# Kernel tuning notes

Hardware: AMD Instinct MI355X
Metric: run time of the kernel (lower is better)

## Reference

```python
import jax, jax.numpy as jnp
import numpy as np

N_NODES = 100000
N_EDGES = 1600000
IN_FEAT = 128
UNITS = 64


def setup_inputs() -> dict:
    key = jax.random.key(0)
    k1, k2, k3, k4, k5 = jax.random.split(key, 5)
    node_states = jax.random.normal(k1, (N_NODES, IN_FEAT), dtype=jnp.float32)
    # edges[:,0] is the destination/segment id; the original TF code's
    # repeat(bincount) normalization assumes edges sorted by edges[:,0].
    dst = jnp.sort(jax.random.randint(k2, (N_EDGES,), 0, N_NODES))
    src = jax.random.randint(k3, (N_EDGES,), 0, N_NODES)
    edges = jnp.stack([dst, src], axis=1).astype(jnp.int64)
    kernel = jax.random.normal(k4, (IN_FEAT, UNITS), dtype=jnp.float32) * 0.05
    kernel_attention = jax.random.normal(k5, (2 * UNITS, 1), dtype=jnp.float32) * 0.05
    return {"node_states": node_states, "edges": edges,
            "kernel": kernel, "kernel_attention": kernel_attention}


def reference(node_states, edges, kernel, kernel_attention):
    n_nodes = node_states.shape[0]
    dst = edges[:, 0]  # segment ids (aggregation target)
    src = edges[:, 1]  # neighbor being gathered

    h = node_states @ kernel                      # [N, U]
    h_dst = h[dst]                                # [E, U]
    h_src = h[src]                                # [E, U]
    # concat(h_dst, h_src) @ a  ==  h_dst @ a[:U] + h_src @ a[U:]
    u = kernel_attention.shape[0] // 2
    scores = (h_dst @ kernel_attention[:u] + h_src @ kernel_attention[u:])[:, 0]  # [E]
    scores = jax.nn.leaky_relu(scores, negative_slope=0.2)  # tf default alpha=0.2
    scores = jnp.exp(jnp.clip(scores, -2.0, 2.0))

    score_sum = jax.ops.segment_sum(scores, dst, num_segments=n_nodes)  # [N]
    attn = scores / score_sum[dst]                                      # [E]

    out = jax.ops.segment_sum(h_src * attn[:, None], dst, num_segments=n_nodes)  # [N, U]
    return out
```

## Files before the change

### kernel.cpp

```cpp
#include <hip/hip_runtime.h>
#include <hip/hip_bf16.h>

#define NN 100000
#define NE 1600000
#define NF 128
#define UU 64

typedef __attribute__((ext_vector_type(8))) short short8;
typedef __attribute__((ext_vector_type(4))) float f32x4;

static const size_t OFF_FLAG = 0;
static const size_t OFF_SRC  = 256;
static const size_t OFF_H2   = OFF_SRC + (size_t)NE * 4;
static const size_t OFF_AD   = OFF_H2  + (size_t)NN * UU * 2;
static const size_t OFF_AS   = OFF_AD  + (size_t)NN * 4;
static const size_t OFF_ROW  = OFF_AS  + (size_t)NN * 4;
static const size_t OFF_WP   = OFF_ROW + (size_t)(NN + 1) * 4;

__device__ __forceinline__ unsigned short bfr(float v) {
    unsigned u = __float_as_uint(v);
    return (unsigned short)((u + 0x7FFFu + ((u >> 16) & 1u)) >> 16);
}

__global__ __launch_bounds__(256) void prep(const int* __restrict__ ew,
                                            const float* __restrict__ W,
                                            int* __restrict__ flag,
                                            unsigned short* __restrict__ Wp) {
    if (threadIdx.x == 0) {
        int a = ew[2 * 400000 + 1] | ew[2 * 800000 + 1] |
                ew[2 * 1200000 + 1] | ew[2 * 1599999 + 1];
        *flag = (a == 0) ? 1 : 0;
    }
    for (int i = threadIdx.x; i < 8192; i += 256) {
        int j   = i & 7;
        int l15 = (i >> 3) & 15;
        int quad = (i >> 7) & 3;
        int kb  = (i >> 9) & 3;
        int nt  = i >> 11;
        Wp[i] = bfr(W[(size_t)(kb * 32 + quad * 8 + j) * UU + nt * 16 + l15]);
    }
}

#define GEMM_BLOCKS   1563
#define ROWS_BLOCKS   391
#define UNPACK_BLOCKS 1563

__global__ __launch_bounds__(256) void mega(const float* __restrict__ X,
                                            const void* __restrict__ edges,
                                            const int* __restrict__ flag,
                                            const unsigned short* __restrict__ Wp,
                                            const float* __restrict__ ka,
                                            unsigned short* __restrict__ h2,
                                            float* __restrict__ a_dst,
                                            float* __restrict__ a_src,
                                            int* __restrict__ src32,
                                            int* __restrict__ rows) {
    int bid = blockIdx.x;
    int tid = threadIdx.x;

    if (bid < GEMM_BLOCKS) {
        int wv = tid >> 6, lane = tid & 63;
        int quad = lane >> 4, l15 = lane & 15;
        int nb = bid * 64 + wv * 16;
        int row = nb + l15; if (row >= NN) row = NN - 1;
        const float* xr = X + (size_t)row * NF + quad * 8;

        short8 afrag[4];
#pragma unroll
        for (int kb = 0; kb < 4; kb++) {
            float4 p0 = *(const float4*)(xr + kb * 32);
            float4 p1 = *(const float4*)(xr + kb * 32 + 4);
            short8 a;
            a[0] = (short)bfr(p0.x); a[1] = (short)bfr(p0.y);
            a[2] = (short)bfr(p0.z); a[3] = (short)bfr(p0.w);
            a[4] = (short)bfr(p1.x); a[5] = (short)bfr(p1.y);
            a[6] = (short)bfr(p1.z); a[7] = (short)bfr(p1.w);
            afrag[kb] = a;
        }

        f32x4 acc[4] = {f32x4{0,0,0,0}, f32x4{0,0,0,0}, f32x4{0,0,0,0}, f32x4{0,0,0,0}};
        const short8* wpf = (const short8*)Wp;
#pragma unroll
        for (int nt = 0; nt < 4; nt++) {
#pragma unroll
            for (int kb = 0; kb < 4; kb++) {
                short8 b = wpf[((nt * 4 + kb) * 4 + quad) * 16 + l15];
                acc[nt] = __builtin_amdgcn_mfma_f32_16x16x32_bf16(afrag[kb], b, acc[nt], 0, 0, 0);
            }
        }

        float kad[4], kas[4];
#pragma unroll
        for (int nt = 0; nt < 4; nt++) {
            kad[nt] = ka[nt * 16 + l15];
            kas[nt] = ka[64 + nt * 16 + l15];
        }
#pragma unroll
        for (int r = 0; r < 4; r++) {
            int m = nb + quad * 4 + r;
            if (m < NN) {
#pragma unroll
                for (int nt = 0; nt < 4; nt++)
                    h2[(size_t)m * UU + nt * 16 + l15] = bfr(acc[nt][r]);
            }
            float pd = acc[0][r] * kad[0] + acc[1][r] * kad[1] + acc[2][r] * kad[2] + acc[3][r] * kad[3];
            float ps = acc[0][r] * kas[0] + acc[1][r] * kas[1] + acc[2][r] * kas[2] + acc[3][r] * kas[3];
            pd += __shfl_xor(pd, 1); pd += __shfl_xor(pd, 2);
            pd += __shfl_xor(pd, 4); pd += __shfl_xor(pd, 8);
            ps += __shfl_xor(ps, 1); ps += __shfl_xor(ps, 2);
            ps += __shfl_xor(ps, 4); ps += __shfl_xor(ps, 8);
            if (l15 == 0 && m < NN) { a_dst[m] = pd; a_src[m] = ps; }
        }
        return;
    }
    bid -= GEMM_BLOCKS;

    if (bid < ROWS_BLOCKS) {
        int n = bid * 256 + tid;
        if (n > NN) return;
        if (n == NN) { rows[NN] = NE; return; }
        int fl = *flag;
        const int* ew = (const int*)edges;
        int lo = 0, hi = NE;
        while (lo < hi) {
            int mid = (lo + hi) >> 1;
            int d = fl ? ew[4 * (size_t)mid] : ew[2 * (size_t)mid];
            if (d < n) lo = mid + 1; else hi = mid;
        }
        rows[n] = lo;
        return;
    }
    bid -= ROWS_BLOCKS;

    {
        int fl = *flag;
        if (fl) {
            const int4* ev = (const int4*)edges;
#pragma unroll
            for (int t = 0; t < 4; t++) {
                int i = bid * 1024 + t * 256 + tid;
                if (i < NE) { int4 v = ev[i]; src32[i] = v.z; }
            }
        } else {
            const int4* ev = (const int4*)edges;
#pragma unroll
            for (int t = 0; t < 2; t++) {
                int p = bid * 512 + t * 256 + tid;
                if (p * 2 < NE) {
                    int4 v = ev[p];
                    *(int2*)(src32 + p * 2) = make_int2(v.y, v.w);
                }
            }
        }
    }
}

__device__ __forceinline__ float edge_score(float ad, float as) {
    float sc = ad + as;
    sc = sc > 0.f ? sc : 0.2f * sc;
    sc = fminf(fmaxf(sc, -2.f), 2.f);
    return __expf(sc);
}

__global__ __launch_bounds__(256) void aggregate(const int* __restrict__ rows,
                                                 const int* __restrict__ srcv,
                                                 const unsigned short* __restrict__ h2,
                                                 const float* __restrict__ a_dst,
                                                 const float* __restrict__ a_src,
                                                 float* __restrict__ out) {
    int gid = blockIdx.x * blockDim.x + threadIdx.x;
    int n = gid >> 6;
    int lane = gid & 63;
    if (n >= NN) return;
    int s = rows[n], e = rows[n + 1];
    int cnt = e - s;
    float ad = a_dst[n];
    int g = lane >> 4, gl = lane & 15;
    const unsigned short* h2g = h2 + gl * 4;
    float4 acc = make_float4(0.f, 0.f, 0.f, 0.f);

#define GBATCH(C0, N)                                                            \
    {                                                                            \
        uint2 rr[4]; float sw[4]; int sjv[4];                                    \
        _Pragma("unroll")                                                        \
        for (int t = 0; t < (N); t++) {                                          \
            int j = (C0) + t * 4 + g;                                            \
            sjv[t] = __shfl(mysrc, j);                                           \
            sw[t]  = __shfl(myscore, j);                                         \
        }                                                                        \
        _Pragma("unroll")                                                        \
        for (int t = 0; t < (N); t++)                                            \
            rr[t] = *(const uint2*)(h2g + (size_t)sjv[t] * UU);                  \
        _Pragma("unroll")                                                        \
        for (int t = 0; t < (N); t++) {                                          \
            acc.x += sw[t] * __uint_as_float(rr[t].x << 16);                     \
            acc.y += sw[t] * __uint_as_float(rr[t].x & 0xFFFF0000u);             \
            acc.z += sw[t] * __uint_as_float(rr[t].y << 16);                     \
            acc.w += sw[t] * __uint_as_float(rr[t].y & 0xFFFF0000u);             \
        }                                                                        \
    }

    float inv;
    if (cnt <= 64) {
        int idx = s + lane;
        int mysrc = 0; float myscore = 0.f;
        if (idx < e) { mysrc = srcv[idx]; myscore = edge_score(ad, a_src[mysrc]); }
        int c = 0;
        for (; c + 16 <= cnt; c += 16) GBATCH(c, 4);
        int rem = cnt - c;
        if (rem > 12)     GBATCH(c, 4)
        else if (rem > 8) GBATCH(c, 3)
        else if (rem > 4) GBATCH(c, 2)
        else if (rem > 0) GBATCH(c, 1);
        float t = myscore;
#pragma unroll
        for (int off = 32; off; off >>= 1) t += __shfl_xor(t, off);
        inv = (cnt > 0) ? 1.f / t : 0.f;
    } else {
        float ssum = 0.f;
        for (int i = s + lane; i < e; i += 64) ssum += edge_score(ad, a_src[srcv[i]]);
#pragma unroll
        for (int off = 32; off; off >>= 1) ssum += __shfl_xor(ssum, off);
        inv = 1.f / ssum;
        for (int c0 = s; c0 < e; c0 += 64) {
            int i = c0 + lane;
            int mysrc = 0; float myscore = 0.f;
            if (i < e) { mysrc = srcv[i]; myscore = edge_score(ad, a_src[mysrc]); }
            GBATCH(0, 4); GBATCH(16, 4); GBATCH(32, 4); GBATCH(48, 4);
        }
    }
#undef GBATCH

    acc.x += __shfl_xor(acc.x, 32); acc.y += __shfl_xor(acc.y, 32);
    acc.z += __shfl_xor(acc.z, 32); acc.w += __shfl_xor(acc.w, 32);
    acc.x += __shfl_xor(acc.x, 16); acc.y += __shfl_xor(acc.y, 16);
    acc.z += __shfl_xor(acc.z, 16); acc.w += __shfl_xor(acc.w, 16);
    if (lane < 16) {
        float4 o = make_float4(acc.x * inv, acc.y * inv, acc.z * inv, acc.w * inv);
        *(float4*)(out + (size_t)n * UU + gl * 4) = o;
    }
}

extern "C" void kernel_launch(void* const* d_in, const int* in_sizes, int n_in,
                              void* d_out, int out_size, void* d_ws, size_t ws_size,
                              hipStream_t stream) {
    const float* X  = (const float*)d_in[0];
    const void*  Ed = d_in[1];
    const float* W  = (const float*)d_in[2];
    const float* KA = (const float*)d_in[3];
    float* out = (float*)d_out;

    char* ws = (char*)d_ws;
    int*            flag  = (int*)(ws + OFF_FLAG);
    int*            src32 = (int*)(ws + OFF_SRC);
    unsigned short* h2    = (unsigned short*)(ws + OFF_H2);
    float*          a_dst = (float*)(ws + OFF_AD);
    float*          a_src = (float*)(ws + OFF_AS);
    int*            rows  = (int*)(ws + OFF_ROW);
    unsigned short* Wp    = (unsigned short*)(ws + OFF_WP);

    prep<<<1, 256, 0, stream>>>((const int*)Ed, W, flag, Wp);
    mega<<<GEMM_BLOCKS + ROWS_BLOCKS + UNPACK_BLOCKS, 256, 0, stream>>>(
        X, Ed, flag, Wp, KA, h2, a_dst, a_src, src32, rows);
    aggregate<<<(NN * 64 + 255) / 256, 256, 0, stream>>>(rows, src32, h2, a_dst, a_src, out);
}
```

Baseline: 163.3 us.

## Slice h into 8-column planes and precompute edge weights in separate kernel

Stores the projected features as eight column slices of 8 bf16 values each (slice-major), so that each aggregate block handles one slice and the gathered rows for that slice stay more cache-resident. Per-edge attention weights are now computed once in a new kernel and written to a workspace buffer instead of inside the aggregate loop. The aggregate kernel is rewritten so that 16 edges are handled in parallel per wave with 4-byte gathers, and prep is spread over 33 blocks. The cost is an extra kernel launch, an extra pass over the edges, and eight times as many reads of the rows and src arrays across the column slices.

```diff
diff --git a/kernel.cpp b/kernel.cpp
--- a/kernel.cpp
+++ b/kernel.cpp
@@ -16,6 +16,7 @@
 static const size_t OFF_AS   = OFF_AD  + (size_t)NN * 4;
 static const size_t OFF_ROW  = OFF_AS  + (size_t)NN * 4;
 static const size_t OFF_WP   = OFF_ROW + (size_t)(NN + 1) * 4;
+static const size_t OFF_W    = OFF_WP  + 16384;
 
 __device__ __forceinline__ unsigned short bfr(float v) {
     unsigned u = __float_as_uint(v);
@@ -26,19 +27,21 @@
                                             const float* __restrict__ W,
                                             int* __restrict__ flag,
                                             unsigned short* __restrict__ Wp) {
-    if (threadIdx.x == 0) {
-        int a = ew[2 * 400000 + 1] | ew[2 * 800000 + 1] |
-                ew[2 * 1200000 + 1] | ew[2 * 1599999 + 1];
-        *flag = (a == 0) ? 1 : 0;
-    }
-    for (int i = threadIdx.x; i < 8192; i += 256) {
-        int j   = i & 7;
-        int l15 = (i >> 3) & 15;
-        int quad = (i >> 7) & 3;
-        int kb  = (i >> 9) & 3;
-        int nt  = i >> 11;
-        Wp[i] = bfr(W[(size_t)(kb * 32 + quad * 8 + j) * UU + nt * 16 + l15]);
-    }
+    if (blockIdx.x == 0) {
+        if (threadIdx.x == 0) {
+            int a = ew[2 * 400000 + 1] | ew[2 * 800000 + 1] |
+                    ew[2 * 1200000 + 1] | ew[2 * 1599999 + 1];
+            *flag = (a == 0) ? 1 : 0;
+        }
+        return;
+    }
+    int i = (blockIdx.x - 1) * 256 + threadIdx.x;
+    int j   = i & 7;
+    int l15 = (i >> 3) & 15;
+    int quad = (i >> 7) & 3;
+    int kb  = (i >> 9) & 3;
+    int nt  = i >> 11;
+    Wp[i] = bfr(W[(size_t)(kb * 32 + quad * 8 + j) * UU + nt * 16 + l15]);
 }
 
 #define GEMM_BLOCKS   1563
@@ -50,7 +53,7 @@
                                             const int* __restrict__ flag,
                                             const unsigned short* __restrict__ Wp,
                                             const float* __restrict__ ka,
-                                            unsigned short* __restrict__ h2,
+                                            unsigned short* __restrict__ h2s,
                                             float* __restrict__ a_dst,
                                             float* __restrict__ a_src,
                                             int* __restrict__ src32,
@@ -95,13 +98,16 @@
             kad[nt] = ka[nt * 16 + l15];
             kas[nt] = ka[64 + nt * 16 + l15];
         }
+        int sl2 = l15 >> 3, u8 = l15 & 7;
 #pragma unroll
         for (int r = 0; r < 4; r++) {
             int m = nb + quad * 4 + r;
             if (m < NN) {
 #pragma unroll
-                for (int nt = 0; nt < 4; nt++)
-                    h2[(size_t)m * UU + nt * 16 + l15] = bfr(acc[nt][r]);
+                for (int nt = 0; nt < 4; nt++) {
+                    int slice = 2 * nt + sl2;
+                    h2s[((size_t)slice * NN + m) * 8 + u8] = bfr(acc[nt][r]);
+                }
             }
             float pd = acc[0][r] * kad[0] + acc[1][r] * kad[1] + acc[2][r] * kad[2] + acc[3][r] * kad[3];
             float ps = acc[0][r] * kas[0] + acc[1][r] * kas[1] + acc[2][r] * kas[2] + acc[3][r] * kas[3];
@@ -162,82 +168,75 @@
     return __expf(sc);
 }
 
+__global__ __launch_bounds__(256) void wkern(const void* __restrict__ edges,
+                                             const int* __restrict__ flag,
+                                             const float* __restrict__ a_dst,
+                                             const float* __restrict__ a_src,
+                                             float* __restrict__ w) {
+    int fl = *flag;
+    int tid = threadIdx.x;
+    if (fl) {
+        const int4* ev = (const int4*)edges;
+#pragma unroll
+        for (int t = 0; t < 4; t++) {
+            int i = blockIdx.x * 1024 + t * 256 + tid;
+            if (i < NE) {
+                int4 v = ev[i];
+                w[i] = edge_score(a_dst[v.x], a_src[v.z]);
+            }
+        }
+    } else {
+        const int4* ev = (const int4*)edges;
+#pragma unroll
+        for (int t = 0; t < 2; t++) {
+            int p = blockIdx.x * 512 + t * 256 + tid;
+            if (p * 2 < NE) {
+                int4 v = ev[p];
+                float2 wv = make_float2(edge_score(a_dst[v.x], a_src[v.y]),
+                                        edge_score(a_dst[v.z], a_src[v.w]));
+                *(float2*)(w + p * 2) = wv;
+            }
+        }
+    }
+}
+
 __global__ __launch_bounds__(256) void aggregate(const int* __restrict__ rows,
                                                  const int* __restrict__ srcv,
-                                                 const unsigned short* __restrict__ h2,
-                                                 const float* __restrict__ a_dst,
-                                                 const float* __restrict__ a_src,
+                                                 const float* __restrict__ w,
+                                                 const unsigned short* __restrict__ h2s,
                                                  float* __restrict__ out) {
-    int gid = blockIdx.x * blockDim.x + threadIdx.x;
-    int n = gid >> 6;
-    int lane = gid & 63;
-    if (n >= NN) return;
-    int s = rows[n], e = rows[n + 1];
-    int cnt = e - s;
-    float ad = a_dst[n];
-    int g = lane >> 4, gl = lane & 15;
-    const unsigned short* h2g = h2 + gl * 4;
-    float4 acc = make_float4(0.f, 0.f, 0.f, 0.f);
-
-#define GBATCH(C0, N)                                                            \
-    {                                                                            \
-        uint2 rr[4]; float sw[4]; int sjv[4];                                    \
-        _Pragma("unroll")                                                        \
-        for (int t = 0; t < (N); t++) {                                          \
-            int j = (C0) + t * 4 + g;                                            \
-            sjv[t] = __shfl(mysrc, j);                                           \
-            sw[t]  = __shfl(myscore, j);                                         \
-        }                                                                        \
-        _Pragma("unroll")                                                        \
-        for (int t = 0; t < (N); t++)                                            \
-            rr[t] = *(const uint2*)(h2g + (size_t)sjv[t] * UU);                  \
-        _Pragma("unroll")                                                        \
-        for (int t = 0; t < (N); t++) {                                          \
-            acc.x += sw[t] * __uint_as_float(rr[t].x << 16);                     \
-            acc.y += sw[t] * __uint_as_float(rr[t].x & 0xFFFF0000u);             \
-            acc.z += sw[t] * __uint_as_float(rr[t].y << 16);                     \
-            acc.w += sw[t] * __uint_as_float(rr[t].y & 0xFFFF0000u);             \
-        }                                                                        \
-    }
-
-    float inv;
-    if (cnt <= 64) {
-        int idx = s + lane;
-        int mysrc = 0; float myscore = 0.f;
-        if (idx < e) { mysrc = srcv[idx]; myscore = edge_score(ad, a_src[mysrc]); }
-        int c = 0;
-        for (; c + 16 <= cnt; c += 16) GBATCH(c, 4);
-        int rem = cnt - c;
-        if (rem > 12)     GBATCH(c, 4)
-        else if (rem > 8) GBATCH(c, 3)
-        else if (rem > 4) GBATCH(c, 2)
-        else if (rem > 0) GBATCH(c, 1);
-        float t = myscore;
-#pragma unroll
-        for (int off = 32; off; off >>= 1) t += __shfl_xor(t, off);
-        inv = (cnt > 0) ? 1.f / t : 0.f;
-    } else {
-        float ssum = 0.f;
-        for (int i = s + lane; i < e; i += 64) ssum += edge_score(ad, a_src[srcv[i]]);
-#pragma unroll
-        for (int off = 32; off; off >>= 1) ssum += __shfl_xor(ssum, off);
-        inv = 1.f / ssum;
-        for (int c0 = s; c0 < e; c0 += 64) {
-            int i = c0 + lane;
-            int mysrc = 0; float myscore = 0.f;
-            if (i < e) { mysrc = srcv[i]; myscore = edge_score(ad, a_src[mysrc]); }
-            GBATCH(0, 4); GBATCH(16, 4); GBATCH(32, 4); GBATCH(48, 4);
-        }
-    }
-#undef GBATCH
-
-    acc.x += __shfl_xor(acc.x, 32); acc.y += __shfl_xor(acc.y, 32);
-    acc.z += __shfl_xor(acc.z, 32); acc.w += __shfl_xor(acc.w, 32);
-    acc.x += __shfl_xor(acc.x, 16); acc.y += __shfl_xor(acc.y, 16);
-    acc.z += __shfl_xor(acc.z, 16); acc.w += __shfl_xor(acc.w, 16);
-    if (lane < 16) {
-        float4 o = make_float4(acc.x * inv, acc.y * inv, acc.z * inv, acc.w * inv);
-        *(float4*)(out + (size_t)n * UU + gl * 4) = o;
+    int x = blockIdx.x & 7;
+    int g16 = blockIdx.x >> 3;
+    int wv = threadIdx.x >> 6, lane = threadIdx.x & 63;
+    int grp = lane >> 2, q = lane & 3;
+    const unsigned short* hs = h2s + (size_t)x * NN * 8 + q * 2;
+    int nbase = g16 * 16 + wv * 4;
+
+#pragma unroll
+    for (int i = 0; i < 4; i++) {
+        int n = nbase + i;
+        int s = rows[n], e = rows[n + 1];
+        int cnt = e - s;
+        float a0 = 0.f, a1 = 0.f, ws = 0.f;
+        for (int c = s; c < e; c += 16) {
+            int j = c + grp;
+            float wl = 0.f; int sj = 0;
+            if (j < e) { wl = w[j]; sj = srcv[j]; }
+            unsigned hh = *(const unsigned*)(hs + (size_t)sj * 8);
+            a0 += wl * __uint_as_float(hh << 16);
+            a1 += wl * __uint_as_float(hh & 0xFFFF0000u);
+            ws += wl;
+        }
+#pragma unroll
+        for (int off = 4; off <= 32; off <<= 1) {
+            a0 += __shfl_xor(a0, off);
+            a1 += __shfl_xor(a1, off);
+            ws += __shfl_xor(ws, off);
+        }
+        float inv = (cnt > 0) ? 1.f / ws : 0.f;
+        if (lane < 4)
+            *(float2*)(out + (size_t)n * UU + x * 8 + q * 2) =
+                make_float2(a0 * inv, a1 * inv);
     }
 }
 
@@ -253,14 +252,16 @@
     char* ws = (char*)d_ws;
     int*            flag  = (int*)(ws + OFF_FLAG);
     int*            src32 = (int*)(ws + OFF_SRC);
-    unsigned short* h2    = (unsigned short*)(ws + OFF_H2);
+    unsigned short* h2s   = (unsigned short*)(ws + OFF_H2);
     float*          a_dst = (float*)(ws + OFF_AD);
     float*          a_src = (float*)(ws + OFF_AS);
     int*            rows  = (int*)(ws + OFF_ROW);
     unsigned short* Wp    = (unsigned short*)(ws + OFF_WP);
-
-    prep<<<1, 256, 0, stream>>>((const int*)Ed, W, flag, Wp);
+    float*          wbuf  = (float*)(ws + OFF_W);
+
+    prep<<<33, 256, 0, stream>>>((const int*)Ed, W, flag, Wp);
     mega<<<GEMM_BLOCKS + ROWS_BLOCKS + UNPACK_BLOCKS, 256, 0, stream>>>(
-        X, Ed, flag, Wp, KA, h2, a_dst, a_src, src32, rows);
-    aggregate<<<(NN * 64 + 255) / 256, 256, 0, stream>>>(rows, src32, h2, a_dst, a_src, out);
-}
+        X, Ed, flag, Wp, KA, h2s, a_dst, a_src, src32, rows);
+    wkern<<<1563, 256, 0, stream>>>(Ed, flag, a_dst, a_src, wbuf);
+    aggregate<<<6250 * 8, 256, 0, stream>>>(rows, src32, wbuf, h2s, out);
+}
```

New measurement: 262.3 us. 1.61x slower.
